# Kernel optimization log

Hardware: AMD Instinct MI355X
Metric: run time of the kernel (lower is better)

## Reference

```python
import jax, jax.numpy as jnp
import numpy as np

KSIZE = 3
KN = (KSIZE - 1) // 2  # 1
TEMP = 50.0


def _extract_patches(x, same_pad):
    """TF tf.image.extract_patches ordering: per location, (dy, dx, channel).
    x: [b,H,W,d] -> [b,h,w,9*d] (h=H,w=W if same_pad else H-2,W-2)."""
    if same_pad:
        x = jnp.pad(x, ((0, 0), (KN, KN), (KN, KN), (0, 0)))
    b, Hp, Wp, d = x.shape
    h, w = Hp - 2 * KN, Wp - 2 * KN
    slices = [x[:, dy:dy + h, dx:dx + w, :]
              for dy in range(KSIZE) for dx in range(KSIZE)]
    return jnp.concatenate(slices, axis=-1)


def setup_inputs() -> dict:
    key = jax.random.key(0)
    k1, k2, k3 = jax.random.split(key, 3)
    b, h, w, dims = 4, 48, 48, 64
    g_in = jax.random.normal(k1, (b, h, w, dims), dtype=jnp.float32)
    # binary inpainting mask (1 = known background, 0 = hole)
    mask = (jax.random.uniform(k2, (b, h, w, 1)) > 0.5).astype(jnp.float32)
    W2 = jax.random.normal(k3, (2 * dims, dims), dtype=jnp.float32) / np.sqrt(2.0 * dims)
    b2 = jnp.zeros((dims,), dtype=jnp.float32)
    return {"g_in": g_in, "mask": mask, "W2": W2, "b2": b2}


def reference(g_in, mask, W2, b2):
    b, h, w, dims = g_in.shape
    c = (h - 2 * KN) * (w - 2 * KN)

    mask_r = mask  # already (h,w,1); broadcasts over dims (== tile)
    bg = g_in * mask_r

    # p1: VALID 3x3 patches of bg -> dynamic kernels, [b, c, 9*dims]
    p1 = _extract_patches(bg, same_pad=False).reshape(b, c, KSIZE * KSIZE * dims)
    # p2: SAME 3x3 patches of g_in, [b, h, w, 9*dims]
    p2 = _extract_patches(g_in, same_pad=True)

    # cross-correlation: conv2d(ft, k1) == per-location dot with each bg patch
    CS = jnp.einsum('byxk,bjk->byxj', p2, p1)              # [b,h,w,c]
    k1d = jnp.sum(p1 * p1, axis=2)                          # [b,c]
    wwd = jnp.sum(p2 * p2, axis=3, keepdims=True)           # [b,h,w,1]
    DS1 = k1d[:, None, None, :] + wwd - 2.0 * CS            # squared distances
    mu = jnp.mean(DS1, axis=3, keepdims=True)
    sd = jnp.std(DS1, axis=3, keepdims=True)                # population std (tf.math.reduce_std)
    DS2 = -jnp.tanh((DS1 - mu) / sd)
    CA = jax.nn.softmax(TEMP * DS2, axis=-1)                # [b,h,w,c]

    # transposed conv aggregation with per-sample kernels k2[b,j,dy,dx,ch]
    k2 = p1.reshape(b, c, KSIZE, KSIZE, dims)
    CA_pad = jnp.pad(CA, ((0, 0), (KN, KN), (KN, KN), (0, 0)))
    acl = jnp.zeros((b, h, w, dims), dtype=g_in.dtype)
    for dy in range(KSIZE):
        for dx in range(KSIZE):
            win = CA_pad[:, 2 * KN - dy:2 * KN - dy + h, 2 * KN - dx:2 * KN - dx + w, :]
            acl = acl + jnp.einsum('byxj,bjd->byxd', win, k2[:, :, dy, dx, :])
    acl = acl / 9.0

    ACL = bg + acl * (1.0 - mask_r)
    con1 = jnp.concatenate([g_in, ACL], axis=3)             # [b,h,w,2*dims]
    return jax.nn.elu(jnp.einsum('byxk,kd->byxd', con1, W2) + b2)
```

## Files before the change

kernel.cpp:

```cpp
#include <hip/hip_runtime.h>
#include <hip/hip_fp16.h>
#include <math.h>

#define BB 4
#define HH 48
#define WW 48
#define DD 64
#define CH 46
#define CWp 46
#define CC (CH*CWp)
#define KK 576
#define HWp (HH*WW)
#define KPAD 2176
#define KSPLIT0 1088
#define PW 50
#define PP (PW*PW)

typedef __attribute__((ext_vector_type(8))) short short8;
typedef __attribute__((ext_vector_type(4))) float float4v;

#define OFFB_GPAD  ((size_t)0)
#define OFFB_BGPAD ((size_t)1280000)
#define OFFB_E     ((size_t)2560000)
#define OFFB_K1D   ((size_t)2596864)
#define OFFB_P1T   ((size_t)2630720)
#define OFFB_S     ((size_t)12657728)
#define OFFB_AGG0  ((size_t)52765760)
#define OFFB_AGG1  ((size_t)63382592)

__device__ __forceinline__ ushort f2bf(float x) {
    unsigned u = __float_as_uint(x);
    return (ushort)((u + 0x7FFFu + ((u >> 16) & 1u)) >> 16);
}

__device__ __forceinline__ float waveReduceSum(float x) {
#pragma unroll
    for (int o = 32; o > 0; o >>= 1) x += __shfl_down(x, o, 64);
    return x;
}

__device__ __forceinline__ float blockReduceSum(float x, float* sm) {
#pragma unroll
    for (int o = 32; o > 0; o >>= 1) x += __shfl_down(x, o, 64);
    int lane = threadIdx.x & 63, w = threadIdx.x >> 6;
    __syncthreads();
    if (lane == 0) sm[w] = x;
    __syncthreads();
    return sm[0] + sm[1] + sm[2] + sm[3];
}

__device__ __forceinline__ float fast_tanh(float z) {
    float e = __expf(2.f * z);
    return 1.f - 2.f / (e + 1.f);
}

typedef __attribute__((address_space(3))) void lds_void_t;
typedef __attribute__((address_space(1))) void gmem_void_t;
__device__ __forceinline__ void gld16(const ushort* g, ushort* lds) {
    __builtin_amdgcn_global_load_lds((gmem_void_t*)g, (lds_void_t*)lds, 16, 0, 0);
}

__global__ __launch_bounds__(256) void build_pads(const float* __restrict__ g,
                                                  const float* __restrict__ mask,
                                                  ushort* __restrict__ gpad,
                                                  ushort* __restrict__ bgpad,
                                                  float* __restrict__ e) {
    int w = threadIdx.x >> 6, c = threadIdx.x & 63;
    int q4 = blockIdx.x * 4 + w;
    int b = q4 / PP, q = q4 % PP;
    int yp = q / PW, xp = q % PW;
    size_t o = (size_t)q4 * DD + c;
    if (yp >= 1 && yp <= HH && xp >= 1 && xp <= WW) {
        int pix = (yp - 1) * WW + (xp - 1);
        float gv = g[((size_t)b * HWp + pix) * DD + c];
        float m  = mask[(size_t)b * HWp + pix];
        float bgv = gv * m;
        gpad[o]  = f2bf(gv);
        bgpad[o] = f2bf(bgv);
        float ss = waveReduceSum(bgv * bgv);
        if (c == 0) e[b * HWp + pix] = ss;
    } else {
        gpad[o] = 0;
        bgpad[o] = 0;
    }
}

__global__ __launch_bounds__(256) void build_p1t_k1d(const ushort* __restrict__ bgpad,
                                                     const float* __restrict__ e,
                                                     ushort* __restrict__ p1t,
                                                     float* __restrict__ k1d) {
    int t = threadIdx.x;
    if (blockIdx.x < BB * KK) {
        int rowid = blockIdx.x;
        int b = rowid / KK, n = rowid % KK;
        int d9 = n >> 6, c = n & 63;
        int dy = d9 / 3, dx = d9 - dy * 3;
        const ushort* src = bgpad + (size_t)b * PP * DD + c;
        ushort* dst = p1t + (size_t)rowid * KPAD;
#pragma unroll
        for (int pass = 0; pass < 2; pass++) {
            int j0;
            if (pass == 0) j0 = t * 8;
            else { if (t >= 16) break; j0 = 2048 + t * 8; }
            ushort v[8];
#pragma unroll
            for (int u = 0; u < 8; u++) {
                int j = j0 + u;
                ushort val = 0;
                if (j < CC) {
                    int jy = j / CWp, jx = j - jy * CWp;
                    val = src[(size_t)((jy + dy + 1) * PW + (jx + dx + 1)) * DD];
                }
                v[u] = val;
            }
            *(uint4*)(dst + j0) = *(const uint4*)v;
        }
    } else {
        int jg = (blockIdx.x - BB * KK) * 256 + t;
        if (jg < BB * CC) {
            int b = jg / CC, j = jg % CC;
            int jy = j / CWp, jx = j - jy * CWp;
            const float* eb = e + b * HWp + jy * WW + jx;
            float s = 0.f;
#pragma unroll
            for (int dy = 0; dy < 3; dy++)
#pragma unroll
                for (int dx = 0; dx < 3; dx++) s += eb[dy * WW + dx];
            k1d[jg] = s;
        }
    }
}

__global__ __launch_bounds__(256) void gemm1_nt(const ushort* __restrict__ gpad,
                                                const ushort* __restrict__ bgpad,
                                                __half* __restrict__ Cout) {
    __shared__ ushort As[2 * 4096];
    __shared__ ushort Bs[2 * 4096];
    int i0 = blockIdx.x;
    int b = (i0 & 7) >> 1;
    int tile = ((i0 >> 3) << 1) | (i0 & 1);
    int ty = tile / 17, tx = tile - ty * 17;
    int m0 = ty * 128, n0 = tx * 128;
    const ushort* Ag = gpad + (size_t)b * PP * DD;
    const ushort* Bg = bgpad + (size_t)b * PP * DD;

    int tid = threadIdx.x;
    int l = tid & 63, w = tid >> 6;
    int quad = l >> 4, l15 = l & 15;
    int sw8 = (l15 >> 1) & 3;
    int wm = (w >> 1) * 64, wn = (w & 1) * 64;
    int rowInC = l >> 2;
    int cSw = (l & 3) ^ ((l >> 3) & 3);

    int baseA[2], baseB[2];
    bool vB[2];
#pragma unroll
    for (int i = 0; i < 2; i++) {
        int rg = w * 2 + i;
        int r = rg * 16 + rowInC;
        int p = m0 + r;
        int y = p / WW, x = p - y * WW;
        baseA[i] = (y * PW + x) * DD + cSw * 8;
        int n = n0 + r;
        vB[i] = (n < CC);
        int jy = 0, jx = 0;
        if (vB[i]) { jy = n / CWp; jx = n - jy * CWp; }
        baseB[i] = ((jy + 1) * PW + (jx + 1)) * DD + cSw * 8;
    }

    float4v acc[4][4];
#pragma unroll
    for (int i = 0; i < 4; i++)
#pragma unroll
        for (int j = 0; j < 4; j++) acc[i][j] = (float4v){0.f, 0.f, 0.f, 0.f};

#pragma unroll
    for (int i = 0; i < 2; i++) {
        int rg = w * 2 + i;
        gld16(Ag + baseA[i], As + rg * 512);
        if (vB[i]) gld16(Bg + baseB[i], Bs + rg * 512);
    }

    int buf = 0;
    for (int k0 = 0; k0 < KK; k0 += 32) {
        __syncthreads();
        int nb = buf ^ 1;
        int kn = k0 + 32;
        if (kn < KK) {
            int d9 = kn >> 6;
            int dy = d9 / 3, dx = d9 - dy * 3;
            int off = (dy * PW + dx) * DD + (kn & 63);
#pragma unroll
            for (int i = 0; i < 2; i++) {
                int rg = w * 2 + i;
                gld16(Ag + baseA[i] + off, As + nb * 4096 + rg * 512);
                if (vB[i]) gld16(Bg + baseB[i] + off, Bs + nb * 4096 + rg * 512);
            }
        }
        const ushort* Ax = As + buf * 4096;
        const ushort* Bx = Bs + buf * 4096;
        short8 af[4], bf[4];
#pragma unroll
        for (int i = 0; i < 4; i++)
            af[i] = *(const short8*)&Ax[(wm + i * 16 + l15) * 32 + ((quad ^ sw8)) * 8];
#pragma unroll
        for (int j = 0; j < 4; j++)
            bf[j] = *(const short8*)&Bx[(wn + j * 16 + l15) * 32 + ((quad ^ sw8)) * 8];
#pragma unroll
        for (int i = 0; i < 4; i++)
#pragma unroll
            for (int j = 0; j < 4; j++)
                acc[i][j] = __builtin_amdgcn_mfma_f32_16x16x32_bf16(af[i], bf[j], acc[i][j], 0, 0, 0);
        buf = nb;
    }

    __half* C = Cout + (size_t)b * HWp * KPAD;
#pragma unroll
    for (int i = 0; i < 4; i++) {
#pragma unroll
        for (int j = 0; j < 4; j++) {
            int n = n0 + wn + j * 16 + l15;
            if (n < CC) {
#pragma unroll
                for (int r = 0; r < 4; r++) {
                    int m = m0 + wm + i * 16 + quad * 4 + r;
                    C[(size_t)m * KPAD + n] = __float2half(acc[i][j][r]);
                }
            }
        }
    }
}

template <int NF, bool NMASK>
__device__ __forceinline__ void gemm_tile_db(const ushort* __restrict__ Ab,
                                             const ushort* __restrict__ Bb,
                                             int lda, int ldb, int kb, int ke,
                                             int Nrem,
                                             ushort* As, ushort* Bs,
                                             float4v (&acc)[4][NF]) {
    constexpr int NBI = NF / 2;
    constexpr int BBUF = 2048 * NBI;
    int tid = threadIdx.x;
    int l = tid & 63, w = tid >> 6;
    int quad = l >> 4, l15 = l & 15;
    int sw8 = (l15 >> 1) & 3;
    int wm = (w >> 1) * 64, wn = (w & 1) * (NF * 16);
    int rowInC = l >> 2;
    int cSw = (l & 3) ^ ((l >> 3) & 3);

#pragma unroll
    for (int i = 0; i < 2; i++) {
        int rg = w * 2 + i;
        gld16(Ab + (size_t)(rg * 16 + rowInC) * lda + kb + cSw * 8, As + rg * 512);
    }
#pragma unroll
    for (int i = 0; i < NBI; i++) {
        int rg = w * NBI + i;
        int r = rg * 16 + rowInC;
        if (!NMASK || r < Nrem)
            gld16(Bb + (size_t)r * ldb + kb + cSw * 8, Bs + rg * 512);
    }

    int buf = 0;
    for (int k0 = kb; k0 < ke; k0 += 32) {
        __syncthreads();
        int nb = buf ^ 1;
        if (k0 + 32 < ke) {
#pragma unroll
            for (int i = 0; i < 2; i++) {
                int rg = w * 2 + i;
                gld16(Ab + (size_t)(rg * 16 + rowInC) * lda + (k0 + 32) + cSw * 8,
                      As + nb * 4096 + rg * 512);
            }
#pragma unroll
            for (int i = 0; i < NBI; i++) {
                int rg = w * NBI + i;
                int r = rg * 16 + rowInC;
                if (!NMASK || r < Nrem)
                    gld16(Bb + (size_t)r * ldb + (k0 + 32) + cSw * 8,
                          Bs + nb * BBUF + rg * 512);
            }
        }
        const ushort* Ax = As + buf * 4096;
        const ushort* Bx = Bs + buf * BBUF;
        short8 af[4], bf[NF];
#pragma unroll
        for (int i = 0; i < 4; i++)
            af[i] = *(const short8*)&Ax[(wm + i * 16 + l15) * 32 + ((quad ^ sw8)) * 8];
#pragma unroll
        for (int j = 0; j < NF; j++)
            bf[j] = *(const short8*)&Bx[(wn + j * 16 + l15) * 32 + ((quad ^ sw8)) * 8];
#pragma unroll
        for (int i = 0; i < 4; i++)
#pragma unroll
            for (int j = 0; j < NF; j++)
                acc[i][j] = __builtin_amdgcn_mfma_f32_16x16x32_bf16(af[i], bf[j], acc[i][j], 0, 0, 0);
        buf = nb;
    }
}

__global__ __launch_bounds__(256) void gemm2_split(const ushort* __restrict__ A,
                                                   const ushort* __restrict__ Bt,
                                                   __half* __restrict__ agg0,
                                                   __half* __restrict__ agg1) {
    __shared__ ushort As[2 * 4096];
    __shared__ ushort Bs[2 * 6144];
    int i0 = blockIdx.x;
    int z = i0 & 7;
    int b = z >> 1, split = z & 1;
    int tile = i0 >> 3;
    int ty = tile / 3, tx = tile - ty * 3;
    int m0 = ty * 128, n0 = tx * 192;
    const ushort* Ab = A + (size_t)b * HWp * KPAD + (size_t)m0 * KPAD;
    const ushort* Bb = Bt + (size_t)b * KK * KPAD + (size_t)n0 * KPAD;
    float4v acc[4][6];
#pragma unroll
    for (int i = 0; i < 4; i++)
#pragma unroll
        for (int j = 0; j < 6; j++) acc[i][j] = (float4v){0.f, 0.f, 0.f, 0.f};

    gemm_tile_db<6, false>(Ab, Bb, KPAD, KPAD, split ? KSPLIT0 : 0,
                           split ? KPAD : KSPLIT0, 192, As, Bs, acc);

    int tid = threadIdx.x;
    int lane = tid & 63, wid = tid >> 6;
    int quad = lane >> 4, l15 = lane & 15;
    int wm = (wid >> 1) * 64, wn = (wid & 1) * 96;
    __half* C = (split ? agg1 : agg0) + (size_t)b * HWp * KK;
#pragma unroll
    for (int i = 0; i < 4; i++) {
#pragma unroll
        for (int j = 0; j < 6; j++) {
            int n = n0 + wn + j * 16 + l15;
#pragma unroll
            for (int r = 0; r < 4; r++) {
                int m = m0 + wm + i * 16 + quad * 4 + r;
                C[(size_t)m * KK + n] = __float2half(acc[i][j][r]);
            }
        }
    }
}

__global__ __launch_bounds__(256) void rowsoft(void* __restrict__ Sbase,
                                               const float* __restrict__ k1d) {
    __shared__ float sm[4];
    size_t row = blockIdx.x;
    int b = (int)(row / HWp);
    const __half* p = (const __half*)Sbase + row * KPAD;
    ushort* wout = (ushort*)Sbase + row * KPAD;
    const float* k1 = k1d + (size_t)b * CC;
    int t = threadIdx.x;
    bool hasx = t < 34;

    uint4 raw = *(const uint4*)(p + t * 8);
    uint rx = hasx ? *(const uint*)(p + 2048 + t * 2) : 0u;
    float v[8], vx[2];
    {
        const __half2* h2 = (const __half2*)&raw;
#pragma unroll
        for (int i = 0; i < 4; i++) {
            float2 f = __half22float2(h2[i]);
            v[2 * i] = f.x; v[2 * i + 1] = f.y;
        }
        __half2 hx = *(__half2*)&rx;
        float2 fx = __half22float2(hx);
        vx[0] = fx.x; vx[1] = fx.y;
    }
    {
        const float* kp = k1 + t * 8;
#pragma unroll
        for (int i = 0; i < 8; i++) v[i] = kp[i] - 2.f * v[i];
        if (hasx) {
            vx[0] = k1[2048 + t * 2] - 2.f * vx[0];
            vx[1] = k1[2048 + t * 2 + 1] - 2.f * vx[1];
        }
    }
    float s = 0.f;
#pragma unroll
    for (int i = 0; i < 8; i++) s += v[i];
    if (hasx) s += vx[0] + vx[1];
    s = blockReduceSum(s, sm);
    float mu = s / (float)CC;
    float vs = 0.f;
#pragma unroll
    for (int i = 0; i < 8; i++) { float d = v[i] - mu; vs += d * d; }
    if (hasx) { float d0 = vx[0] - mu, d1 = vx[1] - mu; vs += d0 * d0 + d1 * d1; }
    vs = blockReduceSum(vs, sm);
    float inv_sd = 1.f / sqrtf(vs / (float)CC);
    float es = 0.f;
#pragma unroll
    for (int i = 0; i < 8; i++) {
        v[i] = __expf(-50.f * fast_tanh((v[i] - mu) * inv_sd));
        es += v[i];
    }
    if (hasx) {
        vx[0] = __expf(-50.f * fast_tanh((vx[0] - mu) * inv_sd));
        vx[1] = __expf(-50.f * fast_tanh((vx[1] - mu) * inv_sd));
        es += vx[0] + vx[1];
    }
    es = blockReduceSum(es, sm);
    float invz = 1.f / es;

    ushort o[8];
#pragma unroll
    for (int i = 0; i < 8; i++) o[i] = f2bf(v[i] * invz);
    *(uint4*)(wout + t * 8) = *(const uint4*)o;
    if (hasx) {
        ushort ox[2] = { f2bf(vx[0] * invz), f2bf(vx[1] * invz) };
        *(uint*)(wout + 2048 + t * 2) = *(const uint*)ox;
    } else {
        *(uint*)(wout + CC + 2 * (t - 34)) = 0u;
    }
}

__global__ __launch_bounds__(256) void final_k(const float* __restrict__ g,
                                               const float* __restrict__ mask,
                                               const __half* __restrict__ agg0,
                                               const __half* __restrict__ agg1,
                                               const float* __restrict__ W2,
                                               const float* __restrict__ b2,
                                               float* __restrict__ out) {
    int w = threadIdx.x >> 6, d = threadIdx.x & 63;
    int pix = blockIdx.x * 4 + w;
    int b = pix / HWp, yx = pix % HWp;
    int y = yx / WW, x = yx % WW;

    __shared__ float con1[4][128];
    float acl = 0.f;
#pragma unroll
    for (int dy = 0; dy < 3; dy++) {
#pragma unroll
        for (int dx = 0; dx < 3; dx++) {
            int yy = y + 1 - dy, xx = x + 1 - dx;
            if (yy >= 0 && yy < HH && xx >= 0 && xx < WW) {
                size_t off = ((size_t)(b * HWp + yy * WW + xx)) * KK + (dy * 3 + dx) * DD + d;
                acl += __half2float(agg0[off]) + __half2float(agg1[off]);
            }
        }
    }
    float m = mask[pix];
    float gv = g[(size_t)pix * DD + d];
    float bgv = gv * m;
    float ACL = bgv + (acl / 9.f) * (1.f - m);
    con1[w][d] = gv;
    con1[w][64 + d] = ACL;
    __syncthreads();
    float accv = b2[d];
#pragma unroll 8
    for (int k = 0; k < 128; k++) accv = fmaf(con1[w][k], W2[k * 64 + d], accv);
    out[(size_t)pix * DD + d] = accv > 0.f ? accv : expm1f(accv);
}

extern "C" void kernel_launch(void* const* d_in, const int* in_sizes, int n_in,
                              void* d_out, int out_size, void* d_ws, size_t ws_size,
                              hipStream_t stream) {
    const float* g    = (const float*)d_in[0];
    const float* mask = (const float*)d_in[1];
    const float* W2   = (const float*)d_in[2];
    const float* b2   = (const float*)d_in[3];
    float* out = (float*)d_out;
    char* ws = (char*)d_ws;

    ushort* gpad  = (ushort*)(ws + OFFB_GPAD);
    ushort* bgpad = (ushort*)(ws + OFFB_BGPAD);
    float*  e     = (float*) (ws + OFFB_E);
    float*  k1d   = (float*) (ws + OFFB_K1D);
    ushort* p1t   = (ushort*)(ws + OFFB_P1T);
    void*   S     = (void*)  (ws + OFFB_S);
    __half* agg0  = (__half*)(ws + OFFB_AGG0);
    __half* agg1  = (__half*)(ws + OFFB_AGG1);

    build_pads<<<BB * PP / 4, 256, 0, stream>>>(g, mask, gpad, bgpad, e);
    build_p1t_k1d<<<BB * KK + 34, 256, 0, stream>>>(bgpad, e, p1t, k1d);

    gemm1_nt<<<dim3(1224), 256, 0, stream>>>(gpad, bgpad, (__half*)S);

    rowsoft<<<BB * HWp, 256, 0, stream>>>(S, k1d);

    gemm2_split<<<dim3(432), 256, 0, stream>>>((const ushort*)S, p1t, agg0, agg1);

    final_k<<<BB * HWp / 4, 256, 0, stream>>>(g, mask, agg0, agg1, W2, b2, out);
}
```

Baseline: 205.4 us.

## Split gemm2 K dimension four ways and transpose p1t through shared memory

```diff
diff --git a/kernel.cpp b/kernel.cpp
--- a/kernel.cpp
+++ b/kernel.cpp
@@ -12,7 +12,7 @@
 #define KK 576
 #define HWp (HH*WW)
 #define KPAD 2176
-#define KSPLIT0 1088
+#define KSPLIT 544
 #define PW 50
 #define PP (PW*PW)
 
@@ -27,6 +27,8 @@
 #define OFFB_S     ((size_t)12657728)
 #define OFFB_AGG0  ((size_t)52765760)
 #define OFFB_AGG1  ((size_t)63382592)
+#define OFFB_AGG2  ((size_t)73999424)
+#define OFFB_AGG3  ((size_t)84616256)
 
 __device__ __forceinline__ ushort f2bf(float x) {
     unsigned u = __float_as_uint(x);
@@ -85,49 +87,55 @@
     }
 }
 
-__global__ __launch_bounds__(256) void build_p1t_k1d(const ushort* __restrict__ bgpad,
-                                                     const float* __restrict__ e,
-                                                     ushort* __restrict__ p1t,
-                                                     float* __restrict__ k1d) {
+__global__ __launch_bounds__(256) void build_p1t(const ushort* __restrict__ bgpad,
+                                                 const float* __restrict__ e,
+                                                 ushort* __restrict__ p1t,
+                                                 float* __restrict__ k1d) {
+    int d9 = blockIdx.y, b = blockIdx.z;
     int t = threadIdx.x;
-    if (blockIdx.x < BB * KK) {
-        int rowid = blockIdx.x;
-        int b = rowid / KK, n = rowid % KK;
-        int d9 = n >> 6, c = n & 63;
-        int dy = d9 / 3, dx = d9 - dy * 3;
-        const ushort* src = bgpad + (size_t)b * PP * DD + c;
-        ushort* dst = p1t + (size_t)rowid * KPAD;
-#pragma unroll
-        for (int pass = 0; pass < 2; pass++) {
-            int j0;
-            if (pass == 0) j0 = t * 8;
-            else { if (t >= 16) break; j0 = 2048 + t * 8; }
-            ushort v[8];
-#pragma unroll
-            for (int u = 0; u < 8; u++) {
-                int j = j0 + u;
-                ushort val = 0;
-                if (j < CC) {
-                    int jy = j / CWp, jx = j - jy * CWp;
-                    val = src[(size_t)((jy + dy + 1) * PW + (jx + dx + 1)) * DD];
-                }
-                v[u] = val;
-            }
-            *(uint4*)(dst + j0) = *(const uint4*)v;
-        }
-    } else {
-        int jg = (blockIdx.x - BB * KK) * 256 + t;
+    if (blockIdx.x == 34) {
+        int jg = (b * 9 + d9) * 256 + t;
         if (jg < BB * CC) {
-            int b = jg / CC, j = jg % CC;
+            int bb = jg / CC, j = jg % CC;
             int jy = j / CWp, jx = j - jy * CWp;
-            const float* eb = e + b * HWp + jy * WW + jx;
+            const float* eb = e + bb * HWp + jy * WW + jx;
             float s = 0.f;
 #pragma unroll
-            for (int dy = 0; dy < 3; dy++)
-#pragma unroll
-                for (int dx = 0; dx < 3; dx++) s += eb[dy * WW + dx];
+            for (int ddy = 0; ddy < 3; ddy++)
+#pragma unroll
+                for (int ddx = 0; ddx < 3; ddx++) s += eb[ddy * WW + ddx];
             k1d[jg] = s;
         }
+        return;
+    }
+    __shared__ ushort T[64 * 65];
+    int jt = blockIdx.x;
+    int dy = d9 / 3, dx = d9 - dy * 3;
+    const ushort* src = bgpad + (size_t)b * PP * DD;
+    int lr = t >> 3, c8 = (t & 7) * 8;
+#pragma unroll
+    for (int pass = 0; pass < 2; pass++) {
+        int r = lr + pass * 32;
+        int j = jt * 64 + r;
+        uint4 d = make_uint4(0, 0, 0, 0);
+        if (j < CC) {
+            int jy = j / CWp, jx = j - jy * CWp;
+            d = *(const uint4*)(src + (size_t)((jy + dy + 1) * PW + (jx + dx + 1)) * DD + c8);
+        }
+        ushort tmp[8];
+        *(uint4*)tmp = d;
+#pragma unroll
+        for (int u = 0; u < 8; u++) T[r * 65 + c8 + u] = tmp[u];
+    }
+    __syncthreads();
+#pragma unroll
+    for (int pass = 0; pass < 2; pass++) {
+        int c = lr + pass * 32;
+        int j8 = (t & 7) * 8;
+        ushort tmp[8];
+#pragma unroll
+        for (int u = 0; u < 8; u++) tmp[u] = T[(j8 + u) * 65 + c];
+        *(uint4*)(p1t + ((size_t)b * KK + d9 * 64 + c) * KPAD + jt * 64 + j8) = *(const uint4*)tmp;
     }
 }
 
@@ -302,13 +310,15 @@
 __global__ __launch_bounds__(256) void gemm2_split(const ushort* __restrict__ A,
                                                    const ushort* __restrict__ Bt,
                                                    __half* __restrict__ agg0,
-                                                   __half* __restrict__ agg1) {
+                                                   __half* __restrict__ agg1,
+                                                   __half* __restrict__ agg2,
+                                                   __half* __restrict__ agg3) {
     __shared__ ushort As[2 * 4096];
     __shared__ ushort Bs[2 * 6144];
     int i0 = blockIdx.x;
-    int z = i0 & 7;
-    int b = z >> 1, split = z & 1;
-    int tile = i0 >> 3;
+    int z = i0 & 15;
+    int b = z >> 2, split = z & 3;
+    int tile = i0 >> 4;
     int ty = tile / 3, tx = tile - ty * 3;
     int m0 = ty * 128, n0 = tx * 192;
     const ushort* Ab = A + (size_t)b * HWp * KPAD + (size_t)m0 * KPAD;
@@ -319,14 +329,15 @@
 #pragma unroll
         for (int j = 0; j < 6; j++) acc[i][j] = (float4v){0.f, 0.f, 0.f, 0.f};
 
-    gemm_tile_db<6, false>(Ab, Bb, KPAD, KPAD, split ? KSPLIT0 : 0,
-                           split ? KPAD : KSPLIT0, 192, As, Bs, acc);
+    int kb = split * KSPLIT;
+    gemm_tile_db<6, false>(Ab, Bb, KPAD, KPAD, kb, kb + KSPLIT, 192, As, Bs, acc);
 
     int tid = threadIdx.x;
     int lane = tid & 63, wid = tid >> 6;
     int quad = lane >> 4, l15 = lane & 15;
     int wm = (wid >> 1) * 64, wn = (wid & 1) * 96;
-    __half* C = (split ? agg1 : agg0) + (size_t)b * HWp * KK;
+    __half* aggp = (split == 0) ? agg0 : (split == 1) ? agg1 : (split == 2) ? agg2 : agg3;
+    __half* C = aggp + (size_t)b * HWp * KK;
 #pragma unroll
     for (int i = 0; i < 4; i++) {
 #pragma unroll
@@ -417,6 +428,8 @@
                                                const float* __restrict__ mask,
                                                const __half* __restrict__ agg0,
                                                const __half* __restrict__ agg1,
+                                               const __half* __restrict__ agg2,
+                                               const __half* __restrict__ agg3,
                                                const float* __restrict__ W2,
                                                const float* __restrict__ b2,
                                                float* __restrict__ out) {
@@ -434,7 +447,8 @@
             int yy = y + 1 - dy, xx = x + 1 - dx;
             if (yy >= 0 && yy < HH && xx >= 0 && xx < WW) {
                 size_t off = ((size_t)(b * HWp + yy * WW + xx)) * KK + (dy * 3 + dx) * DD + d;
-                acl += __half2float(agg0[off]) + __half2float(agg1[off]);
+                acl += __half2float(agg0[off]) + __half2float(agg1[off])
+                     + __half2float(agg2[off]) + __half2float(agg3[off]);
             }
         }
     }
@@ -469,15 +483,17 @@
     void*   S     = (void*)  (ws + OFFB_S);
     __half* agg0  = (__half*)(ws + OFFB_AGG0);
     __half* agg1  = (__half*)(ws + OFFB_AGG1);
+    __half* agg2  = (__half*)(ws + OFFB_AGG2);
+    __half* agg3  = (__half*)(ws + OFFB_AGG3);
 
     build_pads<<<BB * PP / 4, 256, 0, stream>>>(g, mask, gpad, bgpad, e);
-    build_p1t_k1d<<<BB * KK + 34, 256, 0, stream>>>(bgpad, e, p1t, k1d);
+    build_p1t<<<dim3(35, 9, BB), 256, 0, stream>>>(bgpad, e, p1t, k1d);
 
     gemm1_nt<<<dim3(1224), 256, 0, stream>>>(gpad, bgpad, (__half*)S);
 
     rowsoft<<<BB * HWp, 256, 0, stream>>>(S, k1d);
 
-    gemm2_split<<<dim3(432), 256, 0, stream>>>((const ushort*)S, p1t, agg0, agg1);
-
-    final_k<<<BB * HWp / 4, 256, 0, stream>>>(g, mask, agg0, agg1, W2, b2, out);
-}
+    gemm2_split<<<dim3(864), 256, 0, stream>>>((const ushort*)S, p1t, agg0, agg1, agg2, agg3);
+
+    final_k<<<BB * HWp / 4, 256, 0, stream>>>(g, mask, agg0, agg1, agg2, agg3, W2, b2, out);
+}
```

New measurement: 197.4 us. 3.9% less time.
